# Kernel tuning notes

Hardware: AMD Instinct MI355X
Metric: run time of the kernel (lower is better)

## Reference

```python
import jax, jax.numpy as jnp
import numpy as np

B, T, D, H, A = 1, 262144, 8, 64, 4  # batch, seq_len, state_dim, hidden, n_actions


def setup_inputs() -> dict:
    key = jax.random.key(0)
    ks = jax.random.split(key, 10)
    s = lambda k, shape, sc: jax.random.normal(k, shape, dtype=jnp.float32) * sc
    return {
        "x": jax.random.normal(ks[0], (B, T, D), dtype=jnp.float32),
        # encoder MLP (Dense->tanh, Dense->tanh)
        "W1": s(ks[1], (D, H), 0.5), "b1": jnp.zeros((H,), jnp.float32),
        "W2": s(ks[2], (H, H), 0.15), "b2": jnp.zeros((H,), jnp.float32),
        # SimpleRNN params: h_t = tanh(x_t @ Wx + h_{t-1} @ Wh + b_rnn)
        "Wx": s(ks[3], (H, H), 0.15), "Wh": s(ks[4], (H, H), 0.1),
        "b_rnn": jnp.zeros((H,), jnp.float32),
        # means head
        "Wm": s(ks[5], (H, A), 0.01), "bm": jnp.zeros((A,), jnp.float32),
    }


def reference(x, W1, b1, W2, b2, Wx, Wh, b_rnn, Wm, bm):
    # Masking(mask_value=0): a timestep is masked if ALL features == 0
    mask = jnp.any(x != 0.0, axis=-1)  # [B, T] bool
    # TimeDistributed encoder (applies pointwise over time -> plain batched matmul)
    h1 = jnp.tanh(x @ W1 + b1)          # [B, T, H]
    h2 = jnp.tanh(h1 @ W2 + b2)         # [B, T, H]
    # Precompute input contribution to the RNN outside the scan (efficient form)
    xz = h2 @ Wx + b_rnn                # [B, T, H]

    def step(h, inp):
        z, m = inp                       # z: [B, H], m: [B]
        h_new = jnp.tanh(z + h @ Wh)
        # masked timesteps: carry previous state through (Keras RNN masking semantics)
        h = jnp.where(m[:, None], h_new, h)
        return h, h

    h0 = jnp.zeros((B, H), x.dtype)
    _, hs = jax.lax.scan(step, h0, (jnp.swapaxes(xz, 0, 1), jnp.swapaxes(mask, 0, 1)))
    hs = jnp.swapaxes(hs, 0, 1)          # [B, T, H]
    means = hs @ Wm + bm                 # [B, T, A]
    return means
```

## Files before the change

kernel.cpp:

```cpp
#include <hip/hip_runtime.h>
#include <hip/hip_bf16.h>

constexpr int T_LEN  = 262144;
constexpr int H      = 64;
constexpr int S_LEN  = 4;
constexpr int WARM   = 20;
constexpr int CHUNKS = T_LEN / S_LEN;
constexpr int NWAVE  = CHUNKS / 16;
constexpr int PRE_STRIDE = 68;

typedef __attribute__((ext_vector_type(8))) short short8;
typedef __attribute__((ext_vector_type(4))) float f32x4;

__device__ __forceinline__ float fast_tanh(float x) {
    float e = __expf(2.0f * x);
    return 1.0f - 2.0f * __builtin_amdgcn_rcpf(e + 1.0f);
}
__device__ __forceinline__ unsigned short f2bf(float v) {
    unsigned u = __builtin_bit_cast(unsigned, v);
    return (unsigned short)((u + 0x7fffu + ((u >> 16) & 1u)) >> 16);
}
__device__ __forceinline__ float bf2f(unsigned short b) {
    return __builtin_bit_cast(float, (unsigned)b << 16);
}
__device__ __forceinline__ unsigned pack2(float a, float b) {
#if __has_builtin(__builtin_amdgcn_cvt_pk_bf16_f32)
    typedef __attribute__((ext_vector_type(2))) __bf16 bf16x2;
    bf16x2 r = __builtin_amdgcn_cvt_pk_bf16_f32(a, b);
    return __builtin_bit_cast(unsigned, r);
#else
    return (unsigned)f2bf(a) | ((unsigned)f2bf(b) << 16);
#endif
}

__global__ __launch_bounds__(256) void encoder_kernel(
    const float* __restrict__ x,
    const float* __restrict__ W1, const float* __restrict__ b1,
    const float* __restrict__ W2, const float* __restrict__ b2,
    const float* __restrict__ Wx, const float* __restrict__ b_rnn,
    unsigned short* __restrict__ z_s, float* __restrict__ m_s)
{
    __shared__ uint4 w1f[4 * 64];
    __shared__ uint4 w2f[8 * 64];
    __shared__ uint4 w3f[8 * 64];
    __shared__ float pre_[4][16 * PRE_STRIDE];

    const int tid = threadIdx.x;
    const int w   = tid >> 6;
    const int l   = tid & 63;
    const int q   = l >> 4;
    const int l15 = l & 15;

    {
        const int n  = l;
        const int kg = w;
        float v2[16], v3[16];
        #pragma unroll
        for (int kk = 0; kk < 16; ++kk) {
            v2[kk] = W2[(kg * 16 + kk) * 64 + n];
            v3[kk] = Wx[(kg * 16 + kk) * 64 + n];
        }
        const int kh = kg >> 1;
        const int tn = n >> 4;
        #pragma unroll
        for (int s = 0; s < 2; ++s) {
            const int qq   = (2 * kg + s) & 3;
            const int lane = qq * 16 + (n & 15);
            uint4 o2, o3;
            o2.x = pack2(v2[s*8+0], v2[s*8+1]); o2.y = pack2(v2[s*8+2], v2[s*8+3]);
            o2.z = pack2(v2[s*8+4], v2[s*8+5]); o2.w = pack2(v2[s*8+6], v2[s*8+7]);
            o3.x = pack2(v3[s*8+0], v3[s*8+1]); o3.y = pack2(v3[s*8+2], v3[s*8+3]);
            o3.z = pack2(v3[s*8+4], v3[s*8+5]); o3.w = pack2(v3[s*8+6], v3[s*8+7]);
            w2f[(tn * 2 + kh) * 64 + lane] = o2;
            w3f[(tn * 2 + kh) * 64 + lane] = o3;
        }
        uint4 o1 = make_uint4(0, 0, 0, 0);
        if (q < 2) {
            float v1[8];
            #pragma unroll
            for (int j = 0; j < 8; ++j) v1[j] = W1[j * 64 + w * 16 + l15];
            o1.x = pack2(v1[0], v1[1]); o1.y = pack2(v1[2], v1[3]);
            o1.z = pack2(v1[4], v1[5]); o1.w = pack2(v1[6], v1[7]);
        }
        w1f[w * 64 + l] = o1;
    }
    __syncthreads();

    float b1v[4], b2v[4], brv[4];
    #pragma unroll
    for (int tn = 0; tn < 4; ++tn) {
        b1v[tn] = b1[tn * 16 + l15];
        b2v[tn] = b2[tn * 16 + l15];
        brv[tn] = b_rnn[tn * 16 + l15];
    }

    float* mypre = pre_[w];

    float4 xa = make_float4(0.f, 0.f, 0.f, 0.f), xb = xa;
    if (q < 2) {
        const size_t t0 = (size_t)(blockIdx.x * 256 + w * 16 + l15) * 8;
        xa = *(const float4*)(x + t0);
        xb = *(const float4*)(x + t0 + 4);
    }

    #pragma unroll
    for (int it = 0; it < 4; ++it) {
        const int t0w = blockIdx.x * 256 + it * 64 + w * 16;

        float4 na = xa, nb = xb;
        if (it < 3 && q < 2) {
            const size_t tn0 = (size_t)(t0w + 64 + l15) * 8;
            na = *(const float4*)(x + tn0);
            nb = *(const float4*)(x + tn0 + 4);
        }

        short8 a1 = (short8)0;
        if (q < 2) {
            const float xv[8] = {xa.x, xa.y, xa.z, xa.w, xb.x, xb.y, xb.z, xb.w};
            if (q == 0) {
                bool nz = false;
                #pragma unroll
                for (int d = 0; d < 8; ++d) nz = nz || (xv[d] != 0.0f);
                m_s[t0w + l15] = nz ? 1.0f : 0.0f;
                uint4 o;
                o.x = pack2(xv[0], xv[1]); o.y = pack2(xv[2], xv[3]);
                o.z = pack2(xv[4], xv[5]); o.w = pack2(xv[6], xv[7]);
                a1 = __builtin_bit_cast(short8, o);
            } else {
                float lo[8];
                #pragma unroll
                for (int d = 0; d < 8; ++d) lo[d] = xv[d] - bf2f(f2bf(xv[d]));
                uint4 o;
                o.x = pack2(lo[0], lo[1]); o.y = pack2(lo[2], lo[3]);
                o.z = pack2(lo[4], lo[5]); o.w = pack2(lo[6], lo[7]);
                a1 = __builtin_bit_cast(short8, o);
            }
        }

        {
            f32x4 acc[4];
            #pragma unroll
            for (int tn = 0; tn < 4; ++tn)
                acc[tn] = __builtin_amdgcn_mfma_f32_16x16x32_bf16(
                    a1, __builtin_bit_cast(short8, w1f[tn * 64 + l]),
                    (f32x4){0.f, 0.f, 0.f, 0.f}, 0, 0, 0);
            #pragma unroll
            for (int tn = 0; tn < 4; ++tn)
                #pragma unroll
                for (int r = 0; r < 4; ++r)
                    mypre[(q * 4 + r) * PRE_STRIDE + tn * 16 + l15] =
                        fast_tanh(acc[tn][r] + b1v[tn]);
        }
        __builtin_amdgcn_wave_barrier();

        short8 af[2];
        #pragma unroll
        for (int kh = 0; kh < 2; ++kh) {
            const uint4 r0 = *(const uint4*)(mypre + l15 * PRE_STRIDE + kh * 32 + q * 8);
            const uint4 r1 = *(const uint4*)(mypre + l15 * PRE_STRIDE + kh * 32 + q * 8 + 4);
            uint4 p;
            p.x = pack2(__builtin_bit_cast(float, r0.x), __builtin_bit_cast(float, r0.y));
            p.y = pack2(__builtin_bit_cast(float, r0.z), __builtin_bit_cast(float, r0.w));
            p.z = pack2(__builtin_bit_cast(float, r1.x), __builtin_bit_cast(float, r1.y));
            p.w = pack2(__builtin_bit_cast(float, r1.z), __builtin_bit_cast(float, r1.w));
            af[kh] = __builtin_bit_cast(short8, p);
        }
        __builtin_amdgcn_wave_barrier();

        {
            f32x4 acc[4];
            #pragma unroll
            for (int tn = 0; tn < 4; ++tn) {
                f32x4 d = {0.f, 0.f, 0.f, 0.f};
                d = __builtin_amdgcn_mfma_f32_16x16x32_bf16(
                        af[0], __builtin_bit_cast(short8, w2f[(tn * 2 + 0) * 64 + l]), d, 0, 0, 0);
                d = __builtin_amdgcn_mfma_f32_16x16x32_bf16(
                        af[1], __builtin_bit_cast(short8, w2f[(tn * 2 + 1) * 64 + l]), d, 0, 0, 0);
                acc[tn] = d;
            }
            #pragma unroll
            for (int tn = 0; tn < 4; ++tn)
                #pragma unroll
                for (int r = 0; r < 4; ++r)
                    mypre[(q * 4 + r) * PRE_STRIDE + tn * 16 + l15] =
                        fast_tanh(acc[tn][r] + b2v[tn]);
        }
        __builtin_amdgcn_wave_barrier();

        #pragma unroll
        for (int kh = 0; kh < 2; ++kh) {
            const uint4 r0 = *(const uint4*)(mypre + l15 * PRE_STRIDE + kh * 32 + q * 8);
            const uint4 r1 = *(const uint4*)(mypre + l15 * PRE_STRIDE + kh * 32 + q * 8 + 4);
            uint4 p;
            p.x = pack2(__builtin_bit_cast(float, r0.x), __builtin_bit_cast(float, r0.y));
            p.y = pack2(__builtin_bit_cast(float, r0.z), __builtin_bit_cast(float, r0.w));
            p.z = pack2(__builtin_bit_cast(float, r1.x), __builtin_bit_cast(float, r1.y));
            p.w = pack2(__builtin_bit_cast(float, r1.z), __builtin_bit_cast(float, r1.w));
            af[kh] = __builtin_bit_cast(short8, p);
        }
        __builtin_amdgcn_wave_barrier();

        {
            f32x4 acc[4];
            #pragma unroll
            for (int tn = 0; tn < 4; ++tn) {
                f32x4 d = {0.f, 0.f, 0.f, 0.f};
                d = __builtin_amdgcn_mfma_f32_16x16x32_bf16(
                        af[0], __builtin_bit_cast(short8, w3f[(tn * 2 + 0) * 64 + l]), d, 0, 0, 0);
                d = __builtin_amdgcn_mfma_f32_16x16x32_bf16(
                        af[1], __builtin_bit_cast(short8, w3f[(tn * 2 + 1) * 64 + l]), d, 0, 0, 0);
                acc[tn] = d;
            }
            #pragma unroll
            for (int tn = 0; tn < 4; ++tn)
                #pragma unroll
                for (int r = 0; r < 4; ++r)
                    mypre[(q * 4 + r) * PRE_STRIDE + tn * 16 + l15] = acc[tn][r] + brv[tn];
        }
        __builtin_amdgcn_wave_barrier();

        {
            const int ot = l >> 2;
            const int fq = l & 3;
            const float* src = mypre + ot * PRE_STRIDE + fq * 16;
            const uint4 r0 = *(const uint4*)(src + 0);
            const uint4 r1 = *(const uint4*)(src + 4);
            const uint4 r2 = *(const uint4*)(src + 8);
            const uint4 r3 = *(const uint4*)(src + 12);
            uint4 o0, o1;
            o0.x = pack2(__builtin_bit_cast(float, r0.x), __builtin_bit_cast(float, r0.y));
            o0.y = pack2(__builtin_bit_cast(float, r0.z), __builtin_bit_cast(float, r0.w));
            o0.z = pack2(__builtin_bit_cast(float, r1.x), __builtin_bit_cast(float, r1.y));
            o0.w = pack2(__builtin_bit_cast(float, r1.z), __builtin_bit_cast(float, r1.w));
            o1.x = pack2(__builtin_bit_cast(float, r2.x), __builtin_bit_cast(float, r2.y));
            o1.y = pack2(__builtin_bit_cast(float, r2.z), __builtin_bit_cast(float, r2.w));
            o1.z = pack2(__builtin_bit_cast(float, r3.x), __builtin_bit_cast(float, r3.y));
            o1.w = pack2(__builtin_bit_cast(float, r3.z), __builtin_bit_cast(float, r3.w));
            uint4* dst = (uint4*)(z_s + (size_t)(t0w + ot) * 64 + fq * 16);
            dst[0] = o0;
            dst[1] = o1;
        }
        __builtin_amdgcn_wave_barrier();

        xa = na; xb = nb;
    }
}

__global__ __launch_bounds__(256) void rnn_kernel(
    const unsigned short* __restrict__ z_s, const float* __restrict__ m_s,
    const float* __restrict__ Wh, const float* __restrict__ Wm,
    const float* __restrict__ bm, float* __restrict__ out)
{
    __shared__ float pre_[4][16 * PRE_STRIDE];

    const int tid = threadIdx.x;
    const int w   = tid >> 6;
    const int l   = tid & 63;
    const int q   = l >> 4;
    const int l15 = l & 15;
    const int rw  = blockIdx.x * 4 + w;
    const int c   = rw * 16 + l15;

    short8 bfrag[8];
    #pragma unroll
    for (int tn = 0; tn < 4; ++tn) {
        #pragma unroll
        for (int kh = 0; kh < 2; ++kh) {
            short8 s;
            #pragma unroll
            for (int j = 0; j < 8; ++j)
                s[j] = (short)f2bf(Wh[(kh * 32 + q * 8 + j) * 64 + tn * 16 + l15]);
            bfrag[tn * 2 + kh] = s;
        }
    }
    short8 wmf[2];
    #pragma unroll
    for (int kh = 0; kh < 2; ++kh) {
        short8 s;
        #pragma unroll
        for (int j = 0; j < 8; ++j)
            s[j] = (l15 < 4) ? (short)f2bf(Wm[(kh * 32 + q * 8 + j) * 4 + l15]) : (short)0;
        wmf[kh] = s;
    }
    const float bm_l = (l15 < 4) ? bm[l15] : 0.0f;

    short8 hfrag[2];
    hfrag[0] = (short8)0;
    hfrag[1] = (short8)0;
    float* mypre = pre_[w];

    auto t_of = [&](int st) -> size_t {
        long tt = (long)c * S_LEN + st;
        if (tt < 0) tt = 0;
        if (tt >= T_LEN) tt = T_LEN - 1;
        return (size_t)tt;
    };

    uint4 zA0, zA1, zB0, zB1;
    float mA, mB;
    {
        const size_t tA = t_of(-WARM);
        zA0 = *(const uint4*)(z_s + tA * 64 + q * 8);
        zA1 = *(const uint4*)(z_s + tA * 64 + 32 + q * 8);
        mA  = m_s[tA];
        const size_t tB = t_of(-WARM + 1);
        zB0 = *(const uint4*)(z_s + tB * 64 + q * 8);
        zB1 = *(const uint4*)(z_s + tB * 64 + 32 + q * 8);
        mB  = m_s[tB];
    }

    auto body = [&](int st, bool means_prev) {
        const size_t t2 = t_of(st + 2);
        const uint4 zC0 = *(const uint4*)(z_s + t2 * 64 + q * 8);
        const uint4 zC1 = *(const uint4*)(z_s + t2 * 64 + 32 + q * 8);
        const float mC  = m_s[t2];

        if (c * S_LEN + st == 0) { hfrag[0] = (short8)0; hfrag[1] = (short8)0; }

        f32x4 acc[4];
        #pragma unroll
        for (int tn = 0; tn < 4; ++tn) {
            f32x4 d = {0.f, 0.f, 0.f, 0.f};
            d = __builtin_amdgcn_mfma_f32_16x16x32_bf16(hfrag[0], bfrag[tn * 2 + 0], d, 0, 0, 0);
            d = __builtin_amdgcn_mfma_f32_16x16x32_bf16(hfrag[1], bfrag[tn * 2 + 1], d, 0, 0, 0);
            acc[tn] = d;
        }
        if (means_prev) {
            f32x4 a2 = {0.f, 0.f, 0.f, 0.f};
            a2 = __builtin_amdgcn_mfma_f32_16x16x32_bf16(hfrag[0], wmf[0], a2, 0, 0, 0);
            a2 = __builtin_amdgcn_mfma_f32_16x16x32_bf16(hfrag[1], wmf[1], a2, 0, 0, 0);
            if (l15 < 4) {
                #pragma unroll
                for (int r = 0; r < 4; ++r) {
                    const int cm = rw * 16 + q * 4 + r;
                    const size_t tp = (size_t)cm * S_LEN + (st - 1);
                    out[tp * 4 + l15] = a2[r] + bm_l;
                }
            }
        }
        #pragma unroll
        for (int tn = 0; tn < 4; ++tn)
            #pragma unroll
            for (int r = 0; r < 4; ++r)
                mypre[(q * 4 + r) * PRE_STRIDE + tn * 16 + l15] = acc[tn][r];
        __builtin_amdgcn_wave_barrier();

        const uint4 zvv[2] = {zA0, zA1};
        #pragma unroll
        for (int kh = 0; kh < 2; ++kh) {
            const unsigned short* zp = (const unsigned short*)&zvv[kh];
            const uint4 r0 = *(const uint4*)(mypre + l15 * PRE_STRIDE + kh * 32 + q * 8);
            const uint4 r1 = *(const uint4*)(mypre + l15 * PRE_STRIDE + kh * 32 + q * 8 + 4);
            const unsigned pd[8] = {r0.x, r0.y, r0.z, r0.w, r1.x, r1.y, r1.z, r1.w};
            float th[8];
            #pragma unroll
            for (int j = 0; j < 8; ++j)
                th[j] = fast_tanh(__builtin_bit_cast(float, pd[j]) + bf2f(zp[j]));
            uint4 p;
            p.x = pack2(th[0], th[1]); p.y = pack2(th[2], th[3]);
            p.z = pack2(th[4], th[5]); p.w = pack2(th[6], th[7]);
            const short8 ns = __builtin_bit_cast(short8, p);
            hfrag[kh] = (mA != 0.0f) ? ns : hfrag[kh];
        }
        __builtin_amdgcn_wave_barrier();

        zA0 = zB0; zA1 = zB1; mA = mB;
        zB0 = zC0; zB1 = zC1; mB = mC;
    };

    for (int st = -WARM; st < 0; ++st) body(st, false);
    for (int st = 0; st < S_LEN; ++st) body(st, st >= 1);

    {
        f32x4 a2 = {0.f, 0.f, 0.f, 0.f};
        a2 = __builtin_amdgcn_mfma_f32_16x16x32_bf16(hfrag[0], wmf[0], a2, 0, 0, 0);
        a2 = __builtin_amdgcn_mfma_f32_16x16x32_bf16(hfrag[1], wmf[1], a2, 0, 0, 0);
        if (l15 < 4) {
            #pragma unroll
            for (int r = 0; r < 4; ++r) {
                const int cm = rw * 16 + q * 4 + r;
                const size_t tp = (size_t)cm * S_LEN + (S_LEN - 1);
                out[tp * 4 + l15] = a2[r] + bm_l;
            }
        }
    }
}

extern "C" void kernel_launch(void* const* d_in, const int* in_sizes, int n_in,
                              void* d_out, int out_size, void* d_ws, size_t ws_size,
                              hipStream_t stream) {
    const float* x     = (const float*)d_in[0];
    const float* W1    = (const float*)d_in[1];
    const float* b1    = (const float*)d_in[2];
    const float* W2    = (const float*)d_in[3];
    const float* b2    = (const float*)d_in[4];
    const float* Wx    = (const float*)d_in[5];
    const float* Wh    = (const float*)d_in[6];
    const float* b_rnn = (const float*)d_in[7];
    const float* Wm    = (const float*)d_in[8];
    const float* bm    = (const float*)d_in[9];
    float* out = (float*)d_out;

    unsigned short* z_s = (unsigned short*)d_ws;
    float*          m_s = (float*)((char*)d_ws + (size_t)T_LEN * H * 2);

    encoder_kernel<<<T_LEN / 256, 256, 0, stream>>>(x, W1, b1, W2, b2, Wx, b_rnn, z_s, m_s);
    rnn_kernel<<<NWAVE / 4, 256, 0, stream>>>(z_s, m_s, Wh, Wm, bm, out);
}
```

Before: 149.1 us.

## Lengthen RNN chunks, pad z/mask buffers, and double-buffer per-step loads

Chunk length goes from 4 to 8 and warm-up from 20 to 24 steps, so each wave computes more outputs for its warm-up recurrence and redundant warm-up work per output drops. Half as many waves run, each with a longer serial chain, so there is less latency hiding. The z and mask workspace now has WARM padding rows in front and a small tail, which removes the per-step clamp of time indices. Loads use a two-slot ping-pong buffer filled after each step instead of rotating three registers. Reading the uninitialised padding relies on the hidden-state reset at t=0 for the first chunk.

```diff
diff --git a/kernel.cpp b/kernel.cpp
--- a/kernel.cpp
+++ b/kernel.cpp
@@ -3,11 +3,12 @@
 
 constexpr int T_LEN  = 262144;
 constexpr int H      = 64;
-constexpr int S_LEN  = 4;
-constexpr int WARM   = 20;
+constexpr int S_LEN  = 8;
+constexpr int WARM   = 24;
 constexpr int CHUNKS = T_LEN / S_LEN;
 constexpr int NWAVE  = CHUNKS / 16;
 constexpr int PRE_STRIDE = 68;
+constexpr int ZPAD_TAIL = 4;
 
 typedef __attribute__((ext_vector_type(8))) short short8;
 typedef __attribute__((ext_vector_type(4))) float f32x4;
@@ -247,7 +248,7 @@
 }
 
 __global__ __launch_bounds__(256) void rnn_kernel(
-    const unsigned short* __restrict__ z_s, const float* __restrict__ m_s,
+    const unsigned short* __restrict__ z_pad, const float* __restrict__ m_pad,
     const float* __restrict__ Wh, const float* __restrict__ Wm,
     const float* __restrict__ bm, float* __restrict__ out)
 {
@@ -289,34 +290,26 @@
     hfrag[1] = (short8)0;
     float* mypre = pre_[w];
 
-    auto t_of = [&](int st) -> size_t {
-        long tt = (long)c * S_LEN + st;
-        if (tt < 0) tt = 0;
-        if (tt >= T_LEN) tt = T_LEN - 1;
-        return (size_t)tt;
-    };
-
-    uint4 zA0, zA1, zB0, zB1;
-    float mA, mB;
-    {
-        const size_t tA = t_of(-WARM);
-        zA0 = *(const uint4*)(z_s + tA * 64 + q * 8);
-        zA1 = *(const uint4*)(z_s + tA * 64 + 32 + q * 8);
-        mA  = m_s[tA];
-        const size_t tB = t_of(-WARM + 1);
-        zB0 = *(const uint4*)(z_s + tB * 64 + q * 8);
-        zB1 = *(const uint4*)(z_s + tB * 64 + 32 + q * 8);
-        mB  = m_s[tB];
-    }
-
-    auto body = [&](int st, bool means_prev) {
-        const size_t t2 = t_of(st + 2);
-        const uint4 zC0 = *(const uint4*)(z_s + t2 * 64 + q * 8);
-        const uint4 zC1 = *(const uint4*)(z_s + t2 * 64 + 32 + q * 8);
-        const float mC  = m_s[t2];
-
-        if (c * S_LEN + st == 0) { hfrag[0] = (short8)0; hfrag[1] = (short8)0; }
-
+    const unsigned short* zrow = z_pad + (size_t)c * S_LEN * 64;
+    const float*          mrow = m_pad + (size_t)c * S_LEN;
+    const int tneg = -(c * S_LEN);
+
+    uint4 zb0[2], zb1[2];
+    float mb0, mb1;
+    zb0[0] = *(const uint4*)(zrow + q * 8);
+    zb0[1] = *(const uint4*)(zrow + 32 + q * 8);
+    mb0    = mrow[0];
+    zb1[0] = *(const uint4*)(zrow + 64 + q * 8);
+    zb1[1] = *(const uint4*)(zrow + 64 + 32 + q * 8);
+    mb1    = mrow[1];
+    zrow += 128; mrow += 2;
+
+    auto body = [&](uint4* zbuf, float& mref,
+                    const unsigned short* zrl, const float* mrl,
+                    int stv, bool means_prev, bool may_reset) {
+        if (may_reset && rw == 0) {
+            if (stv == tneg) { hfrag[0] = (short8)0; hfrag[1] = (short8)0; }
+        }
         f32x4 acc[4];
         #pragma unroll
         for (int tn = 0; tn < 4; ++tn) {
@@ -333,7 +326,7 @@
                 #pragma unroll
                 for (int r = 0; r < 4; ++r) {
                     const int cm = rw * 16 + q * 4 + r;
-                    const size_t tp = (size_t)cm * S_LEN + (st - 1);
+                    const size_t tp = (size_t)cm * S_LEN + (stv - 1);
                     out[tp * 4 + l15] = a2[r] + bm_l;
                 }
             }
@@ -345,10 +338,9 @@
                 mypre[(q * 4 + r) * PRE_STRIDE + tn * 16 + l15] = acc[tn][r];
         __builtin_amdgcn_wave_barrier();
 
-        const uint4 zvv[2] = {zA0, zA1};
         #pragma unroll
         for (int kh = 0; kh < 2; ++kh) {
-            const unsigned short* zp = (const unsigned short*)&zvv[kh];
+            const unsigned short* zp = (const unsigned short*)&zbuf[kh];
             const uint4 r0 = *(const uint4*)(mypre + l15 * PRE_STRIDE + kh * 32 + q * 8);
             const uint4 r1 = *(const uint4*)(mypre + l15 * PRE_STRIDE + kh * 32 + q * 8 + 4);
             const unsigned pd[8] = {r0.x, r0.y, r0.z, r0.w, r1.x, r1.y, r1.z, r1.w};
@@ -360,16 +352,29 @@
             p.x = pack2(th[0], th[1]); p.y = pack2(th[2], th[3]);
             p.z = pack2(th[4], th[5]); p.w = pack2(th[6], th[7]);
             const short8 ns = __builtin_bit_cast(short8, p);
-            hfrag[kh] = (mA != 0.0f) ? ns : hfrag[kh];
-        }
-        __builtin_amdgcn_wave_barrier();
-
-        zA0 = zB0; zA1 = zB1; mA = mB;
-        zB0 = zC0; zB1 = zC1; mB = mC;
+            hfrag[kh] = (mref != 0.0f) ? ns : hfrag[kh];
+        }
+        __builtin_amdgcn_wave_barrier();
+
+        zbuf[0] = *(const uint4*)(zrl + q * 8);
+        zbuf[1] = *(const uint4*)(zrl + 32 + q * 8);
+        mref    = mrl[0];
     };
 
-    for (int st = -WARM; st < 0; ++st) body(st, false);
-    for (int st = 0; st < S_LEN; ++st) body(st, st >= 1);
+    for (int i = 0; i < WARM / 2; ++i) {
+        const int st = -WARM + 2 * i;
+        body(zb0, mb0, zrow,      mrow,     st,     false, true);
+        body(zb1, mb1, zrow + 64, mrow + 1, st + 1, false, true);
+        zrow += 128; mrow += 2;
+    }
+
+    #pragma unroll
+    for (int st = 0; st < S_LEN; ++st) {
+        if ((st & 1) == 0)
+            body(zb0, mb0, zrow + st * 64, mrow + st, st, st >= 1, st == 0);
+        else
+            body(zb1, mb1, zrow + st * 64, mrow + st, st, true, false);
+    }
 
     {
         f32x4 a2 = {0.f, 0.f, 0.f, 0.f};
@@ -401,9 +406,13 @@
     const float* bm    = (const float*)d_in[9];
     float* out = (float*)d_out;
 
-    unsigned short* z_s = (unsigned short*)d_ws;
-    float*          m_s = (float*)((char*)d_ws + (size_t)T_LEN * H * 2);
+    unsigned short* z_pad = (unsigned short*)d_ws;
+    const size_t z_rows   = (size_t)(WARM + T_LEN + ZPAD_TAIL);
+    float*          m_pad = (float*)((char*)d_ws + z_rows * H * 2);
+
+    unsigned short* z_s = z_pad + (size_t)WARM * H;
+    float*          m_s = m_pad + WARM;
 
     encoder_kernel<<<T_LEN / 256, 256, 0, stream>>>(x, W1, b1, W2, b2, Wx, b_rnn, z_s, m_s);
-    rnn_kernel<<<NWAVE / 4, 256, 0, stream>>>(z_s, m_s, Wh, Wm, bm, out);
-}
+    rnn_kernel<<<NWAVE / 4, 256, 0, stream>>>(z_pad, m_pad, Wh, Wm, bm, out);
+}
```

Measured after the change: 136.8 us. 8.3% less time.
